# Optimization experiments

Measured on AMD Instinct MI355X. Metric: run time of the kernel, lower is better.

Reference implementation:

```python
import jax, jax.numpy as jnp
import numpy as np

N, E, NNZ, CIN, COUT = 100000, 25000, 1600000, 256, 256


def setup_inputs() -> dict:
    key = jax.random.key(0)
    k_x, k_v, k_e, k_w = jax.random.split(key, 4)
    X = jax.random.normal(k_x, (N, CIN), dtype=jnp.float32)
    v_idx = jax.random.randint(k_v, (NNZ,), 0, N)      # vertex of each incidence pair
    e_idx = jax.random.randint(k_e, (NNZ,), 0, E)      # hyperedge of each incidence pair
    # kaiming_normal_ on theta.weight: std = sqrt(2 / fan_in)
    W = jax.random.normal(k_w, (CIN, COUT), dtype=jnp.float32) * np.sqrt(2.0 / CIN)
    b = jnp.zeros((COUT,), dtype=jnp.float32)
    return {"X": X, "W": W, "b": b, "v_idx": v_idx, "e_idx": e_idx}


def reference(X, W, b, v_idx, e_idx):
    # theta: linear projection
    Xp = X @ W + b  # [N, COUT]

    # degrees (edge weights = 1)
    ones = jnp.ones((NNZ,), dtype=Xp.dtype)
    dv = jax.ops.segment_sum(ones, v_idx, num_segments=N)  # vertex degree
    de = jax.ops.segment_sum(ones, e_idx, num_segments=E)  # hyperedge degree
    dv_isqrt = jnp.where(dv > 0, jax.lax.rsqrt(jnp.maximum(dv, 1.0)), 0.0)
    de_inv = jnp.where(de > 0, 1.0 / jnp.maximum(de, 1.0), 0.0)

    # smoothing_with_HGNN: D_v^{-1/2} H D_e^{-1} H^T D_v^{-1/2} Xp
    Xs = Xp * dv_isqrt[:, None]                                            # [N, C]
    Ye = jax.ops.segment_sum(Xs[v_idx], e_idx, num_segments=E) * de_inv[:, None]  # [E, C]
    Zv = jax.ops.segment_sum(Ye[e_idx], v_idx, num_segments=N) * dv_isqrt[:, None]  # [N, C]

    # not is_last: ReLU; bn is None (use_bn=False); dropout identity at eval
    return jax.nn.relu(Zv)
```

## Files before the change

kernel.cpp:

```cpp
#include <hip/hip_runtime.h>
#include <hip/hip_bf16.h>

#define NV 100000
#define NE 25000
#define NNZ_ 1600000
#define CH 256
#define ESTRIDE 128
#define VSTRIDE 48

typedef unsigned int u32;
typedef unsigned short u16;

__device__ __forceinline__ float bf2f(u16 u){ return __uint_as_float(((u32)u)<<16); }
__device__ __forceinline__ u16 f2bf(float f){ __hip_bfloat16 h = __float2bfloat16(f); return *reinterpret_cast<u16*>(&h); }
__device__ __forceinline__ void fma4(float4& a, float s, float4 w){
  a.x = fmaf(s,w.x,a.x); a.y = fmaf(s,w.y,a.y); a.z = fmaf(s,w.z,a.z); a.w = fmaf(s,w.w,a.w);
}
__device__ __forceinline__ void acc4(float4& a, ushort4 u){
  a.x += bf2f(u.x); a.y += bf2f(u.y); a.z += bf2f(u.z); a.w += bf2f(u.w);
}

__global__ void k_build(const int* __restrict__ v_idx, const int* __restrict__ e_idx,
                        int* __restrict__ dv_cnt, int* __restrict__ de_cnt,
                        int* __restrict__ v_listP, int* __restrict__ e_listP){
  int part = blockIdx.x & 7;
  int grp  = blockIdx.x >> 3;
  int ngrp = gridDim.x >> 3;
  int eLo = part*(NE/8), eHi = eLo + (NE/8);
  int vLo = part*(NV/8), vHi = vLo + (NV/8);
  int i = grp*blockDim.x + threadIdx.x;
  int stride = ngrp*blockDim.x;
  for (; i<NNZ_; i+=stride){
    int v = __builtin_nontemporal_load(&v_idx[i]);
    int e = __builtin_nontemporal_load(&e_idx[i]);
    if (e>=eLo && e<eHi){ int s = atomicAdd(&de_cnt[e],1); e_listP[(e<<7)+s] = v; }
    if (v>=vLo && v<vHi){ int s = atomicAdd(&dv_cnt[v],1); v_listP[v*VSTRIDE+s] = e; }
  }
}

__global__ void k_dvis(const int* __restrict__ dv_cnt, float* __restrict__ dv_isqrt){
  int v = blockIdx.x*blockDim.x + threadIdx.x;
  if (v < NV){ int d = dv_cnt[v]; dv_isqrt[v] = d>0 ? rsqrtf((float)d) : 0.f; }
}

__global__ void k_xs(const float4* __restrict__ X4, const float* __restrict__ dv_isqrt,
                     ushort4* __restrict__ Xs4){
  int i = blockIdx.x*blockDim.x + threadIdx.x;
  int v = i >> 6;
  float w = dv_isqrt[v];
  float4 x = X4[i];
  ushort4 o;
  o.x = f2bf(x.x*w); o.y = f2bf(x.y*w); o.z = f2bf(x.z*w); o.w = f2bf(x.w*w);
  Xs4[i] = o;
}

__global__ __launch_bounds__(256) void k_tb(const int* __restrict__ de_cnt, const int* __restrict__ e_listP,
                                            const float* __restrict__ dv_isqrt, float* __restrict__ tb){
  int e = blockIdx.x*4 + (threadIdx.x>>6);
  if (e>=NE) return;
  int lane = threadIdx.x & 63;
  int deg = de_cnt[e];
  int base = e<<7;
  float s = 0.f;
  for (int m=lane; m<deg; m+=64) s += dv_isqrt[e_listP[base+m]];
  #pragma unroll
  for (int d=32; d; d>>=1) s += __shfl_xor(s, d, 64);
  if (lane==0) tb[e] = deg>0 ? s/(float)deg : 0.f;
}

__global__ __launch_bounds__(256) void k_te(const int* __restrict__ de_cnt, const int* __restrict__ e_listP,
                     const ushort4* __restrict__ Xs4, float4* __restrict__ Te4){
  int e = blockIdx.x*4 + (threadIdx.x>>6);
  if (e >= NE) return;
  int lane = threadIdx.x & 63;
  int deg = de_cnt[e];
  int base = e<<7;
  float4 a0 = make_float4(0,0,0,0), a1 = make_float4(0,0,0,0);
  int m = 0;
  for (; m+8 <= deg; m += 8){
    int v0=e_listP[base+m+0], v1=e_listP[base+m+1], v2=e_listP[base+m+2], v3=e_listP[base+m+3];
    int v4=e_listP[base+m+4], v5=e_listP[base+m+5], v6=e_listP[base+m+6], v7=e_listP[base+m+7];
    ushort4 u0=Xs4[(v0<<6)+lane], u1=Xs4[(v1<<6)+lane], u2=Xs4[(v2<<6)+lane], u3=Xs4[(v3<<6)+lane];
    ushort4 u4=Xs4[(v4<<6)+lane], u5=Xs4[(v5<<6)+lane], u6=Xs4[(v6<<6)+lane], u7=Xs4[(v7<<6)+lane];
    acc4(a0,u0); acc4(a1,u1); acc4(a0,u2); acc4(a1,u3);
    acc4(a0,u4); acc4(a1,u5); acc4(a0,u6); acc4(a1,u7);
  }
  for (; m<deg; ++m){
    int v = e_listP[base+m];
    ushort4 u = Xs4[(v<<6)+lane];
    acc4(a0,u);
  }
  float4 acc;
  acc.x=a0.x+a1.x; acc.y=a0.y+a1.y; acc.z=a0.z+a1.z; acc.w=a0.w+a1.w;
  float dinv = deg>0 ? 1.f/(float)deg : 0.f;
  acc.x*=dinv; acc.y*=dinv; acc.z*=dinv; acc.w*=dinv;
  Te4[(e<<6)+lane] = acc;
}

__global__ __launch_bounds__(256) void k_gemm(const float4* __restrict__ Te4, const float4* __restrict__ W4,
                      ushort4* __restrict__ Ue4){
  __shared__ float lds[64][16];
  int t = threadIdx.x;
  int rg = t>>6;
  int cl = t&63;
  int rowBase = blockIdx.x*64;
  float4 acc[16];
  #pragma unroll
  for (int r=0;r<16;r++) acc[r] = make_float4(0,0,0,0);

  for (int kc=0; kc<256; kc+=16){
    int lr = t>>2;
    int lk = (t&3)<<2;
    int gr = rowBase + lr;
    float4 tv = make_float4(0,0,0,0);
    if (gr < NE) tv = Te4[gr*64 + ((kc+lk)>>2)];
    __syncthreads();
    *reinterpret_cast<float4*>(&lds[lr][lk]) = tv;
    __syncthreads();
    float4 w[16];
    #pragma unroll
    for (int kk=0;kk<16;kk++) w[kk] = W4[(kc+kk)*64 + cl];
    #pragma unroll
    for (int r=0;r<16;r++){
      #pragma unroll
      for (int kq=0;kq<4;kq++){
        float4 te = *reinterpret_cast<const float4*>(&lds[rg*16+r][kq<<2]);
        fma4(acc[r], te.x, w[(kq<<2)+0]);
        fma4(acc[r], te.y, w[(kq<<2)+1]);
        fma4(acc[r], te.z, w[(kq<<2)+2]);
        fma4(acc[r], te.w, w[(kq<<2)+3]);
      }
    }
  }
  #pragma unroll
  for (int r=0;r<16;r++){
    int gr = rowBase + rg*16 + r;
    if (gr < NE){
      ushort4 o;
      o.x=f2bf(acc[r].x); o.y=f2bf(acc[r].y); o.z=f2bf(acc[r].z); o.w=f2bf(acc[r].w);
      Ue4[gr*64 + cl] = o;
    }
  }
}

__global__ __launch_bounds__(256) void k_zv(const int* __restrict__ dv_cnt, const int* __restrict__ v_listP,
                    const ushort4* __restrict__ Ue4, const float* __restrict__ tb,
                    const float* __restrict__ dv_isqrt, const float4* __restrict__ b4,
                    float4* __restrict__ out4){
  int v = blockIdx.x*4 + (threadIdx.x>>6);
  if (v >= NV) return;
  int lane = threadIdx.x & 63;
  int deg = dv_cnt[v];
  int base = v*VSTRIDE;
  float4 a0 = make_float4(0,0,0,0), a1 = make_float4(0,0,0,0);
  float sb0 = 0.f, sb1 = 0.f;
  int m = 0;
  for (; m+8 <= deg; m += 8){
    int e0=v_listP[base+m+0], e1=v_listP[base+m+1], e2=v_listP[base+m+2], e3=v_listP[base+m+3];
    int e4=v_listP[base+m+4], e5=v_listP[base+m+5], e6=v_listP[base+m+6], e7=v_listP[base+m+7];
    ushort4 u0=Ue4[(e0<<6)+lane], u1=Ue4[(e1<<6)+lane], u2=Ue4[(e2<<6)+lane], u3=Ue4[(e3<<6)+lane];
    ushort4 u4=Ue4[(e4<<6)+lane], u5=Ue4[(e5<<6)+lane], u6=Ue4[(e6<<6)+lane], u7=Ue4[(e7<<6)+lane];
    acc4(a0,u0); acc4(a1,u1); acc4(a0,u2); acc4(a1,u3);
    acc4(a0,u4); acc4(a1,u5); acc4(a0,u6); acc4(a1,u7);
    sb0 += tb[e0]+tb[e2]+tb[e4]+tb[e6];
    sb1 += tb[e1]+tb[e3]+tb[e5]+tb[e7];
  }
  for (; m<deg; ++m){
    int e = v_listP[base+m];
    ushort4 u = Ue4[(e<<6)+lane];
    acc4(a0,u);
    sb0 += tb[e];
  }
  float4 acc;
  acc.x=a0.x+a1.x; acc.y=a0.y+a1.y; acc.z=a0.z+a1.z; acc.w=a0.w+a1.w;
  float w = dv_isqrt[v];
  float sw = (sb0+sb1)*w;
  float4 bb = b4[lane];
  float4 o;
  o.x = fmaxf(0.f, fmaf(sw, bb.x, acc.x*w));
  o.y = fmaxf(0.f, fmaf(sw, bb.y, acc.y*w));
  o.z = fmaxf(0.f, fmaf(sw, bb.z, acc.z*w));
  o.w = fmaxf(0.f, fmaf(sw, bb.w, acc.w*w));
  out4[(v<<6)+lane] = o;
}

extern "C" void kernel_launch(void* const* d_in, const int* in_sizes, int n_in,
                              void* d_out, int out_size, void* d_ws, size_t ws_size,
                              hipStream_t stream) {
  const float* X = (const float*)d_in[0];
  const float* W = (const float*)d_in[1];
  const float* b = (const float*)d_in[2];
  const int* v_idx = (const int*)d_in[3];
  const int* e_idx = (const int*)d_in[4];
  float* out = (float*)d_out;

  char* p = (char*)d_ws;
  auto alloc = [&](size_t bytes)->void*{
    void* r = (void*)p; p += (bytes + 255) & ~(size_t)255; return r;
  };
  int* dv_cnt     = (int*)alloc((size_t)NV*4);
  int* de_cnt     = (int*)alloc((size_t)NE*4);
  float* dv_isqrt = (float*)alloc((size_t)NV*4);
  float* tb       = (float*)alloc((size_t)NE*4);
  int* e_listP    = (int*)alloc((size_t)NE*ESTRIDE*4);
  int* v_listP    = (int*)alloc((size_t)NV*VSTRIDE*4);
  float* Te       = (float*)alloc((size_t)NE*CH*4);
  u16* Ue         = (u16*)e_listP;
  u16* Xs         = (u16*)d_out;

  hipMemsetAsync(dv_cnt, 0, (size_t)NV*4, stream);
  hipMemsetAsync(de_cnt, 0, (size_t)NE*4, stream);

  k_build<<<1024,256,0,stream>>>(v_idx,e_idx,dv_cnt,de_cnt,v_listP,e_listP);
  k_dvis<<<(NV+255)/256,256,0,stream>>>(dv_cnt, dv_isqrt);
  k_xs<<<(NV*64)/256,256,0,stream>>>((const float4*)X, dv_isqrt, (ushort4*)Xs);
  k_tb<<<(NE+3)/4,256,0,stream>>>(de_cnt,e_listP,dv_isqrt,tb);
  k_te<<<(NE+3)/4,256,0,stream>>>(de_cnt,e_listP,(const ushort4*)Xs,(float4*)Te);
  k_gemm<<<(NE+63)/64,256,0,stream>>>((const float4*)Te,(const float4*)W,(ushort4*)Ue);
  k_zv<<<(NV+3)/4,256,0,stream>>>(dv_cnt,v_listP,(const ushort4*)Ue,tb,dv_isqrt,(const float4*)b,(float4*)out);
}
```

Baseline: 461.6 us.

## Partition incidence build by XCC ID with dynamic chunk tickets and u16 vertex lists

The build kernel now picks its hyperedge and vertex partition from the hardware XCC ID instead of the block index. Blocks pull 4096-element chunks of the incidence arrays from a per-XCC ticket counter. The aim is to keep each partition's atomics and list writes inside one XCC's L2 while balancing load dynamically. Vertex incidence lists are stored as 16-bit hyperedge indices to halve their footprint, which relies on NE fitting in u16. It also assumes all eight XCCs get blocks; if some XCC gets none, its partition is never built.

```diff
diff --git a/kernel.cpp b/kernel.cpp
--- a/kernel.cpp
+++ b/kernel.cpp
@@ -7,6 +7,7 @@
 #define CH 256
 #define ESTRIDE 128
 #define VSTRIDE 48
+#define CHUNK 4096
 
 typedef unsigned int u32;
 typedef unsigned short u16;
@@ -20,21 +21,30 @@
   a.x += bf2f(u.x); a.y += bf2f(u.y); a.z += bf2f(u.z); a.w += bf2f(u.w);
 }
 
-__global__ void k_build(const int* __restrict__ v_idx, const int* __restrict__ e_idx,
+__global__ __launch_bounds__(256) void k_build(const int* __restrict__ v_idx, const int* __restrict__ e_idx,
                         int* __restrict__ dv_cnt, int* __restrict__ de_cnt,
-                        int* __restrict__ v_listP, int* __restrict__ e_listP){
-  int part = blockIdx.x & 7;
-  int grp  = blockIdx.x >> 3;
-  int ngrp = gridDim.x >> 3;
-  int eLo = part*(NE/8), eHi = eLo + (NE/8);
-  int vLo = part*(NV/8), vHi = vLo + (NV/8);
-  int i = grp*blockDim.x + threadIdx.x;
-  int stride = ngrp*blockDim.x;
-  for (; i<NNZ_; i+=stride){
-    int v = __builtin_nontemporal_load(&v_idx[i]);
-    int e = __builtin_nontemporal_load(&e_idx[i]);
-    if (e>=eLo && e<eHi){ int s = atomicAdd(&de_cnt[e],1); e_listP[(e<<7)+s] = v; }
-    if (v>=vLo && v<vHi){ int s = atomicAdd(&dv_cnt[v],1); v_listP[v*VSTRIDE+s] = e; }
+                        u16* __restrict__ v_listP, int* __restrict__ e_listP,
+                        int* __restrict__ tickets){
+  u32 xcc;
+  asm volatile("s_getreg_b32 %0, hwreg(HW_REG_XCC_ID)" : "=s"(xcc));
+  xcc &= 7;
+  int eLo = xcc*(NE/8), eHi = eLo + (NE/8);
+  int vLo = xcc*(NV/8), vHi = vLo + (NV/8);
+  __shared__ int s_chunk;
+  for(;;){
+    __syncthreads();
+    if (threadIdx.x==0) s_chunk = atomicAdd(&tickets[xcc], 1);
+    __syncthreads();
+    long base = (long)s_chunk * CHUNK;
+    if (base >= NNZ_) break;
+    int nel = (int)min((long)CHUNK, (long)NNZ_ - base);
+    for (int k = threadIdx.x; k < nel; k += 256){
+      long i = base + k;
+      int v = __builtin_nontemporal_load(&v_idx[i]);
+      int e = __builtin_nontemporal_load(&e_idx[i]);
+      if (e>=eLo && e<eHi){ int s = atomicAdd(&de_cnt[e],1); e_listP[(e<<7)+s] = v; }
+      if (v>=vLo && v<vHi){ int s = atomicAdd(&dv_cnt[v],1); v_listP[v*VSTRIDE+s] = (u16)e; }
+    }
   }
 }
 
@@ -143,7 +153,7 @@
   }
 }
 
-__global__ __launch_bounds__(256) void k_zv(const int* __restrict__ dv_cnt, const int* __restrict__ v_listP,
+__global__ __launch_bounds__(256) void k_zv(const int* __restrict__ dv_cnt, const u16* __restrict__ v_listP,
                     const ushort4* __restrict__ Ue4, const float* __restrict__ tb,
                     const float* __restrict__ dv_isqrt, const float4* __restrict__ b4,
                     float4* __restrict__ out4){
@@ -202,16 +212,18 @@
   int* de_cnt     = (int*)alloc((size_t)NE*4);
   float* dv_isqrt = (float*)alloc((size_t)NV*4);
   float* tb       = (float*)alloc((size_t)NE*4);
+  int* tickets    = (int*)alloc(8*4);
   int* e_listP    = (int*)alloc((size_t)NE*ESTRIDE*4);
-  int* v_listP    = (int*)alloc((size_t)NV*VSTRIDE*4);
+  u16* v_listP    = (u16*)alloc((size_t)NV*VSTRIDE*2);
   float* Te       = (float*)alloc((size_t)NE*CH*4);
   u16* Ue         = (u16*)e_listP;
   u16* Xs         = (u16*)d_out;
 
   hipMemsetAsync(dv_cnt, 0, (size_t)NV*4, stream);
   hipMemsetAsync(de_cnt, 0, (size_t)NE*4, stream);
-
-  k_build<<<1024,256,0,stream>>>(v_idx,e_idx,dv_cnt,de_cnt,v_listP,e_listP);
+  hipMemsetAsync(tickets, 0, 8*4, stream);
+
+  k_build<<<1024,256,0,stream>>>(v_idx,e_idx,dv_cnt,de_cnt,v_listP,e_listP,tickets);
   k_dvis<<<(NV+255)/256,256,0,stream>>>(dv_cnt, dv_isqrt);
   k_xs<<<(NV*64)/256,256,0,stream>>>((const float4*)X, dv_isqrt, (ushort4*)Xs);
   k_tb<<<(NE+3)/4,256,0,stream>>>(de_cnt,e_listP,dv_isqrt,tb);
```

New measurement: 488.0 us. +5.7%, slower.

## Fuse edge gather with bf16 MFMA GEMM and restructure vertex scatter

Applied to the files above, without the earlier changes.

Fuses the edge-degree bias sum, the edge gather and the W projection into one kernel. The gathered edge rows are kept as bf16 in LDS and multiplied on MFMA 16x16x32 bf16 instructions against a pre-transposed bf16 copy of W, which removes the fp32 Te round trip through global memory and the scalar FMA GEMM. The vertex edge lists now store edge ids as 16-bit values, and the vertex kernel assigns 16 threads per vertex over four channel chunks. This adds bf16 rounding of the edge features and weights, and the vertex kernel now gathers the bias term redundantly in each chunk.

```diff
diff --git a/kernel.cpp b/kernel.cpp
--- a/kernel.cpp
+++ b/kernel.cpp
@@ -7,22 +7,22 @@
 #define CH 256
 #define ESTRIDE 128
 #define VSTRIDE 48
+#define LDSK 264
 
 typedef unsigned int u32;
 typedef unsigned short u16;
+typedef __attribute__((ext_vector_type(8))) short bf16x8;
+typedef __attribute__((ext_vector_type(4))) float f32x4;
 
 __device__ __forceinline__ float bf2f(u16 u){ return __uint_as_float(((u32)u)<<16); }
 __device__ __forceinline__ u16 f2bf(float f){ __hip_bfloat16 h = __float2bfloat16(f); return *reinterpret_cast<u16*>(&h); }
-__device__ __forceinline__ void fma4(float4& a, float s, float4 w){
-  a.x = fmaf(s,w.x,a.x); a.y = fmaf(s,w.y,a.y); a.z = fmaf(s,w.z,a.z); a.w = fmaf(s,w.w,a.w);
-}
 __device__ __forceinline__ void acc4(float4& a, ushort4 u){
   a.x += bf2f(u.x); a.y += bf2f(u.y); a.z += bf2f(u.z); a.w += bf2f(u.w);
 }
 
 __global__ void k_build(const int* __restrict__ v_idx, const int* __restrict__ e_idx,
                         int* __restrict__ dv_cnt, int* __restrict__ de_cnt,
-                        int* __restrict__ v_listP, int* __restrict__ e_listP){
+                        u16* __restrict__ v_listP, int* __restrict__ e_listP){
   int part = blockIdx.x & 7;
   int grp  = blockIdx.x >> 3;
   int ngrp = gridDim.x >> 3;
@@ -34,7 +34,7 @@
     int v = __builtin_nontemporal_load(&v_idx[i]);
     int e = __builtin_nontemporal_load(&e_idx[i]);
     if (e>=eLo && e<eHi){ int s = atomicAdd(&de_cnt[e],1); e_listP[(e<<7)+s] = v; }
-    if (v>=vLo && v<vHi){ int s = atomicAdd(&dv_cnt[v],1); v_listP[v*VSTRIDE+s] = e; }
+    if (v>=vLo && v<vHi){ int s = atomicAdd(&dv_cnt[v],1); v_listP[v*VSTRIDE+s] = (u16)e; }
   }
 }
 
@@ -54,134 +54,127 @@
   Xs4[i] = o;
 }
 
-__global__ __launch_bounds__(256) void k_tb(const int* __restrict__ de_cnt, const int* __restrict__ e_listP,
-                                            const float* __restrict__ dv_isqrt, float* __restrict__ tb){
-  int e = blockIdx.x*4 + (threadIdx.x>>6);
-  if (e>=NE) return;
-  int lane = threadIdx.x & 63;
-  int deg = de_cnt[e];
-  int base = e<<7;
-  float s = 0.f;
-  for (int m=lane; m<deg; m+=64) s += dv_isqrt[e_listP[base+m]];
+__global__ void k_wh(const float* __restrict__ W, u16* __restrict__ Wh){
+  __shared__ float tile[16][17];
+  int bx=blockIdx.x, by=blockIdx.y;
+  int tx=threadIdx.x, ty=threadIdx.y;
+  tile[ty][tx] = W[(by*16+ty)*256 + bx*16+tx];
+  __syncthreads();
+  Wh[(bx*16+ty)*256 + by*16+tx] = f2bf(tile[tx][ty]);
+}
+
+__global__ __launch_bounds__(256) void k_tegemm(const int* __restrict__ de_cnt,
+                     const int* __restrict__ e_listP, const ushort4* __restrict__ Xs4,
+                     const float* __restrict__ dv_isqrt, const u16* __restrict__ Wh,
+                     float* __restrict__ tb, u16* __restrict__ Ue){
+  __shared__ u16 lds[16][LDSK];
+  int t = threadIdx.x, w = t>>6, lane = t&63;
+  int e0 = blockIdx.x*16;
+
+  for (int j=0;j<4;++j){
+    int e = e0 + w*4 + j;
+    int r = w*4 + j;
+    float4 a0=make_float4(0,0,0,0), a1=make_float4(0,0,0,0);
+    float ts = 0.f;
+    if (e < NE){
+      int deg = de_cnt[e], base = e<<7;
+      int m = 0;
+      for (; m+8 <= deg; m += 8){
+        int v0=e_listP[base+m+0], v1=e_listP[base+m+1], v2=e_listP[base+m+2], v3=e_listP[base+m+3];
+        int v4=e_listP[base+m+4], v5=e_listP[base+m+5], v6=e_listP[base+m+6], v7=e_listP[base+m+7];
+        ushort4 u0=Xs4[(v0<<6)+lane], u1=Xs4[(v1<<6)+lane], u2=Xs4[(v2<<6)+lane], u3=Xs4[(v3<<6)+lane];
+        ushort4 u4=Xs4[(v4<<6)+lane], u5=Xs4[(v5<<6)+lane], u6=Xs4[(v6<<6)+lane], u7=Xs4[(v7<<6)+lane];
+        acc4(a0,u0); acc4(a1,u1); acc4(a0,u2); acc4(a1,u3);
+        acc4(a0,u4); acc4(a1,u5); acc4(a0,u6); acc4(a1,u7);
+        ts += dv_isqrt[v0]+dv_isqrt[v1]+dv_isqrt[v2]+dv_isqrt[v3]
+            + dv_isqrt[v4]+dv_isqrt[v5]+dv_isqrt[v6]+dv_isqrt[v7];
+      }
+      for (; m<deg; ++m){
+        int v = e_listP[base+m];
+        ushort4 u = Xs4[(v<<6)+lane];
+        acc4(a0,u);
+        ts += dv_isqrt[v];
+      }
+      float dinv = deg>0 ? 1.f/(float)deg : 0.f;
+      a0.x=(a0.x+a1.x)*dinv; a0.y=(a0.y+a1.y)*dinv; a0.z=(a0.z+a1.z)*dinv; a0.w=(a0.w+a1.w)*dinv;
+      if (lane==0) tb[e] = ts*dinv;
+    }
+    ushort4 o;
+    o.x=f2bf(a0.x); o.y=f2bf(a0.y); o.z=f2bf(a0.z); o.w=f2bf(a0.w);
+    *reinterpret_cast<ushort4*>(&lds[r][lane*4]) = o;
+  }
+  __syncthreads();
+
+  int rr = lane & 15, kg = lane >> 4;
+  f32x4 acc0={0,0,0,0}, acc1={0,0,0,0}, acc2={0,0,0,0}, acc3={0,0,0,0};
   #pragma unroll
-  for (int d=32; d; d>>=1) s += __shfl_xor(s, d, 64);
-  if (lane==0) tb[e] = deg>0 ? s/(float)deg : 0.f;
-}
-
-__global__ __launch_bounds__(256) void k_te(const int* __restrict__ de_cnt, const int* __restrict__ e_listP,
-                     const ushort4* __restrict__ Xs4, float4* __restrict__ Te4){
-  int e = blockIdx.x*4 + (threadIdx.x>>6);
-  if (e >= NE) return;
-  int lane = threadIdx.x & 63;
-  int deg = de_cnt[e];
-  int base = e<<7;
-  float4 a0 = make_float4(0,0,0,0), a1 = make_float4(0,0,0,0);
-  int m = 0;
-  for (; m+8 <= deg; m += 8){
-    int v0=e_listP[base+m+0], v1=e_listP[base+m+1], v2=e_listP[base+m+2], v3=e_listP[base+m+3];
-    int v4=e_listP[base+m+4], v5=e_listP[base+m+5], v6=e_listP[base+m+6], v7=e_listP[base+m+7];
-    ushort4 u0=Xs4[(v0<<6)+lane], u1=Xs4[(v1<<6)+lane], u2=Xs4[(v2<<6)+lane], u3=Xs4[(v3<<6)+lane];
-    ushort4 u4=Xs4[(v4<<6)+lane], u5=Xs4[(v5<<6)+lane], u6=Xs4[(v6<<6)+lane], u7=Xs4[(v7<<6)+lane];
-    acc4(a0,u0); acc4(a1,u1); acc4(a0,u2); acc4(a1,u3);
-    acc4(a0,u4); acc4(a1,u5); acc4(a0,u6); acc4(a1,u7);
-  }
-  for (; m<deg; ++m){
-    int v = e_listP[base+m];
-    ushort4 u = Xs4[(v<<6)+lane];
-    acc4(a0,u);
-  }
-  float4 acc;
-  acc.x=a0.x+a1.x; acc.y=a0.y+a1.y; acc.z=a0.z+a1.z; acc.w=a0.w+a1.w;
-  float dinv = deg>0 ? 1.f/(float)deg : 0.f;
-  acc.x*=dinv; acc.y*=dinv; acc.z*=dinv; acc.w*=dinv;
-  Te4[(e<<6)+lane] = acc;
-}
-
-__global__ __launch_bounds__(256) void k_gemm(const float4* __restrict__ Te4, const float4* __restrict__ W4,
-                      ushort4* __restrict__ Ue4){
-  __shared__ float lds[64][16];
-  int t = threadIdx.x;
-  int rg = t>>6;
-  int cl = t&63;
-  int rowBase = blockIdx.x*64;
-  float4 acc[16];
+  for (int s=0; s<8; ++s){
+    bf16x8 a = *reinterpret_cast<bf16x8*>(&lds[rr][s*32 + kg*8]);
+    const u16* wb = &Wh[(size_t)((w*4)*16 + rr)*256 + s*32 + kg*8];
+    bf16x8 b0 = *reinterpret_cast<const bf16x8*>(wb);
+    bf16x8 b1 = *reinterpret_cast<const bf16x8*>(wb + 16*256);
+    bf16x8 b2 = *reinterpret_cast<const bf16x8*>(wb + 32*256);
+    bf16x8 b3 = *reinterpret_cast<const bf16x8*>(wb + 48*256);
+    acc0 = __builtin_amdgcn_mfma_f32_16x16x32_bf16(a, b0, acc0, 0,0,0);
+    acc1 = __builtin_amdgcn_mfma_f32_16x16x32_bf16(a, b1, acc1, 0,0,0);
+    acc2 = __builtin_amdgcn_mfma_f32_16x16x32_bf16(a, b2, acc2, 0,0,0);
+    acc3 = __builtin_amdgcn_mfma_f32_16x16x32_bf16(a, b3, acc3, 0,0,0);
+  }
+  __syncthreads();
   #pragma unroll
-  for (int r=0;r<16;r++) acc[r] = make_float4(0,0,0,0);
-
-  for (int kc=0; kc<256; kc+=16){
-    int lr = t>>2;
-    int lk = (t&3)<<2;
-    int gr = rowBase + lr;
-    float4 tv = make_float4(0,0,0,0);
-    if (gr < NE) tv = Te4[gr*64 + ((kc+lk)>>2)];
-    __syncthreads();
-    *reinterpret_cast<float4*>(&lds[lr][lk]) = tv;
-    __syncthreads();
-    float4 w[16];
-    #pragma unroll
-    for (int kk=0;kk<16;kk++) w[kk] = W4[(kc+kk)*64 + cl];
-    #pragma unroll
-    for (int r=0;r<16;r++){
-      #pragma unroll
-      for (int kq=0;kq<4;kq++){
-        float4 te = *reinterpret_cast<const float4*>(&lds[rg*16+r][kq<<2]);
-        fma4(acc[r], te.x, w[(kq<<2)+0]);
-        fma4(acc[r], te.y, w[(kq<<2)+1]);
-        fma4(acc[r], te.z, w[(kq<<2)+2]);
-        fma4(acc[r], te.w, w[(kq<<2)+3]);
-      }
-    }
-  }
-  #pragma unroll
-  for (int r=0;r<16;r++){
-    int gr = rowBase + rg*16 + r;
-    if (gr < NE){
-      ushort4 o;
-      o.x=f2bf(acc[r].x); o.y=f2bf(acc[r].y); o.z=f2bf(acc[r].z); o.w=f2bf(acc[r].w);
-      Ue4[gr*64 + cl] = o;
-    }
-  }
-}
-
-__global__ __launch_bounds__(256) void k_zv(const int* __restrict__ dv_cnt, const int* __restrict__ v_listP,
+  for (int reg=0; reg<4; ++reg){
+    int row = kg*4 + reg;
+    lds[row][(w*4+0)*16 + rr] = f2bf(acc0[reg]);
+    lds[row][(w*4+1)*16 + rr] = f2bf(acc1[reg]);
+    lds[row][(w*4+2)*16 + rr] = f2bf(acc2[reg]);
+    lds[row][(w*4+3)*16 + rr] = f2bf(acc3[reg]);
+  }
+  __syncthreads();
+  int orow = t>>4, oseg = t&15;
+  int e = e0 + orow;
+  if (e < NE){
+    uint4 d0 = *reinterpret_cast<uint4*>(&lds[orow][oseg*16]);
+    uint4 d1 = *reinterpret_cast<uint4*>(&lds[orow][oseg*16+8]);
+    *reinterpret_cast<uint4*>(&Ue[(size_t)e*256 + oseg*16])     = d0;
+    *reinterpret_cast<uint4*>(&Ue[(size_t)e*256 + oseg*16 + 8]) = d1;
+  }
+}
+
+__global__ __launch_bounds__(256) void k_zv(const int* __restrict__ dv_cnt, const u16* __restrict__ v_listP,
                     const ushort4* __restrict__ Ue4, const float* __restrict__ tb,
                     const float* __restrict__ dv_isqrt, const float4* __restrict__ b4,
                     float4* __restrict__ out4){
-  int v = blockIdx.x*4 + (threadIdx.x>>6);
-  if (v >= NV) return;
-  int lane = threadIdx.x & 63;
+  const int nvb = NV/16;
+  int chunk = blockIdx.x / nvb;
+  int vb    = blockIdx.x % nvb;
+  int g  = threadIdx.x >> 4;
+  int lc = threadIdx.x & 15;
+  int v = vb*16 + g;
   int deg = dv_cnt[v];
   int base = v*VSTRIDE;
+  float w = dv_isqrt[v];
+  float sb = 0.f;
+  for (int m=0; m<deg; ++m) sb += tb[v_listP[base+m]];
+  float sw = sb*w;
+  int coff = chunk*16 + lc;
   float4 a0 = make_float4(0,0,0,0), a1 = make_float4(0,0,0,0);
-  float sb0 = 0.f, sb1 = 0.f;
   int m = 0;
-  for (; m+8 <= deg; m += 8){
+  for (; m+4 <= deg; m += 4){
     int e0=v_listP[base+m+0], e1=v_listP[base+m+1], e2=v_listP[base+m+2], e3=v_listP[base+m+3];
-    int e4=v_listP[base+m+4], e5=v_listP[base+m+5], e6=v_listP[base+m+6], e7=v_listP[base+m+7];
-    ushort4 u0=Ue4[(e0<<6)+lane], u1=Ue4[(e1<<6)+lane], u2=Ue4[(e2<<6)+lane], u3=Ue4[(e3<<6)+lane];
-    ushort4 u4=Ue4[(e4<<6)+lane], u5=Ue4[(e5<<6)+lane], u6=Ue4[(e6<<6)+lane], u7=Ue4[(e7<<6)+lane];
+    ushort4 u0=Ue4[(e0<<6)+coff], u1=Ue4[(e1<<6)+coff], u2=Ue4[(e2<<6)+coff], u3=Ue4[(e3<<6)+coff];
     acc4(a0,u0); acc4(a1,u1); acc4(a0,u2); acc4(a1,u3);
-    acc4(a0,u4); acc4(a1,u5); acc4(a0,u6); acc4(a1,u7);
-    sb0 += tb[e0]+tb[e2]+tb[e4]+tb[e6];
-    sb1 += tb[e1]+tb[e3]+tb[e5]+tb[e7];
   }
   for (; m<deg; ++m){
     int e = v_listP[base+m];
-    ushort4 u = Ue4[(e<<6)+lane];
-    acc4(a0,u);
-    sb0 += tb[e];
-  }
-  float4 acc;
-  acc.x=a0.x+a1.x; acc.y=a0.y+a1.y; acc.z=a0.z+a1.z; acc.w=a0.w+a1.w;
-  float w = dv_isqrt[v];
-  float sw = (sb0+sb1)*w;
-  float4 bb = b4[lane];
+    acc4(a0, Ue4[(e<<6)+coff]);
+  }
+  float4 bb = b4[coff];
   float4 o;
-  o.x = fmaxf(0.f, fmaf(sw, bb.x, acc.x*w));
-  o.y = fmaxf(0.f, fmaf(sw, bb.y, acc.y*w));
-  o.z = fmaxf(0.f, fmaf(sw, bb.z, acc.z*w));
-  o.w = fmaxf(0.f, fmaf(sw, bb.w, acc.w*w));
-  out4[(v<<6)+lane] = o;
+  o.x = fmaxf(0.f, fmaf(sw, bb.x, (a0.x+a1.x)*w));
+  o.y = fmaxf(0.f, fmaf(sw, bb.y, (a0.y+a1.y)*w));
+  o.z = fmaxf(0.f, fmaf(sw, bb.z, (a0.z+a1.z)*w));
+  o.w = fmaxf(0.f, fmaf(sw, bb.w, (a0.w+a1.w)*w));
+  out4[(v<<6)+coff] = o;
 }
 
 extern "C" void kernel_launch(void* const* d_in, const int* in_sizes, int n_in,
@@ -203,9 +196,9 @@
   float* dv_isqrt = (float*)alloc((size_t)NV*4);
   float* tb       = (float*)alloc((size_t)NE*4);
   int* e_listP    = (int*)alloc((size_t)NE*ESTRIDE*4);
-  int* v_listP    = (int*)alloc((size_t)NV*VSTRIDE*4);
-  float* Te       = (float*)alloc((size_t)NE*CH*4);
-  u16* Ue         = (u16*)e_listP;
+  u16* v_listP    = (u16*)alloc((size_t)NV*VSTRIDE*2);
+  u16* Wh         = (u16*)alloc((size_t)CH*CH*2);
+  u16* Ue         = (u16*)alloc((size_t)NE*CH*2);
   u16* Xs         = (u16*)d_out;
 
   hipMemsetAsync(dv_cnt, 0, (size_t)NV*4, stream);
@@ -214,8 +207,7 @@
   k_build<<<1024,256,0,stream>>>(v_idx,e_idx,dv_cnt,de_cnt,v_listP,e_listP);
   k_dvis<<<(NV+255)/256,256,0,stream>>>(dv_cnt, dv_isqrt);
   k_xs<<<(NV*64)/256,256,0,stream>>>((const float4*)X, dv_isqrt, (ushort4*)Xs);
-  k_tb<<<(NE+3)/4,256,0,stream>>>(de_cnt,e_listP,dv_isqrt,tb);
-  k_te<<<(NE+3)/4,256,0,stream>>>(de_cnt,e_listP,(const ushort4*)Xs,(float4*)Te);
-  k_gemm<<<(NE+63)/64,256,0,stream>>>((const float4*)Te,(const float4*)W,(ushort4*)Ue);
-  k_zv<<<(NV+3)/4,256,0,stream>>>(dv_cnt,v_listP,(const ushort4*)Ue,tb,dv_isqrt,(const float4*)b,(float4*)out);
-}
+  k_wh<<<dim3(16,16),dim3(16,16),0,stream>>>(W, Wh);
+  k_tegemm<<<(NE+15)/16,256,0,stream>>>(de_cnt,e_listP,(const ushort4*)Xs,dv_isqrt,Wh,tb,Ue);
+  k_zv<<<(NV/16)*4,256,0,stream>>>(dv_cnt,v_listP,(const ushort4*)Ue,tb,dv_isqrt,(const float4*)b,(float4*)out);
+}
```

Result: slower. 546.2 us (+18.3%).
